# Kernel tuning notes

Hardware: AMD Instinct MI355X
Metric: run time of the kernel (lower is better)

## Reference

```python
import jax, jax.numpy as jnp
import numpy as np

B, F, D = 4096, 32, 32
LAYER_SIZE = [128, 128]


def setup_inputs() -> dict:
    key = jax.random.key(0)
    k1, k2, k3 = jax.random.split(key, 3)
    inputs = jax.random.normal(k1, (B, F, D), dtype=jnp.float32)
    # CIN filters: shape [1, field_nums[0]*field_nums[i], field_nums[i+1]]
    field_nums = [F] + LAYER_SIZE
    filter_0 = (jax.random.normal(k2, (1, field_nums[0] * field_nums[0], field_nums[1]), dtype=jnp.float32) * 0.05)
    filter_1 = (jax.random.normal(k3, (1, field_nums[0] * field_nums[1], field_nums[2]), dtype=jnp.float32) * 0.05)
    return {"inputs": inputs, "filter_0": filter_0, "filter_1": filter_1}


def _cin_forward(inputs, filters):
    x0 = inputs          # [B, F, D] -- hidden_nn_layers[0]
    prev = inputs        # hidden_nn_layers[-1]
    outs = []
    for W in filters:    # W: [1, F*M, N]
        # outer product over field dims: [B, F, M, D]
        z = jnp.einsum('bhd,bmd->bhmd', x0, prev)
        b, h, m, d = z.shape
        z = z.reshape(b, h * m, d)                 # [B, F*M, D]
        # 1x1 conv over the F*M axis == contraction with W[0]: [F*M, N]
        cur = jnp.einsum('bpd,pn->bnd', z, W[0])   # [B, N, D]
        cur = jax.nn.relu(cur)
        prev = cur
        outs.append(cur)
    result = jnp.concatenate(outs, axis=1)         # [B, sum(layer_size), D]
    return jnp.sum(result, axis=-1)                # [B, sum(layer_size)]


def reference(inputs, filter_0, filter_1):
    return _cin_forward(inputs, (filter_0, filter_1))
```

## Files before the change

### kernel.cpp

```cpp
#include <hip/hip_runtime.h>


typedef _Float16 half_t;
typedef _Float16 half4v __attribute__((ext_vector_type(4)));
typedef _Float16 half8 __attribute__((ext_vector_type(8)));
typedef float f32x16 __attribute__((ext_vector_type(16)));

__global__ void prep_w_kernel(const float* __restrict__ W0,
                              const float* __restrict__ W1,
                              half_t* __restrict__ Wp0,
                              half_t* __restrict__ Wp1) {
  int gid = blockIdx.x * 256 + threadIdx.x;
  int n = gid & 127;
  int tg = (gid >> 7) & 1;
  int s = gid >> 8;
  const float* W;
  half_t* Wp;
  int M, sl;
  if (s < 64) { W = W0; Wp = Wp0; M = 32; sl = s; }
  else        { W = W1; Wp = Wp1; M = 128; sl = s - 64; }
  int h = sl & 31, mc = sl >> 5;
  int kbase = h * M + mc * 16 + tg * 8;
  half8 v;
#pragma unroll
  for (int j = 0; j < 8; ++j) v[j] = (half_t)W[(size_t)(kbase + j) * 128 + n];
  *(half8*)(Wp + ((size_t)(sl * 2 + tg) * 128 + n) * 8) = v;
}

__device__ __forceinline__ int pswz(int row, int m) {
  return row * 128 + (((m >> 3) ^ (row & 15)) << 3) + (m & 7);
}

__device__ __forceinline__ f32x16 mfma3216(half8 a, half8 b, f32x16 c) {
  return __builtin_amdgcn_mfma_f32_32x32x16_f16(a, b, c, 0, 0, 0);
}

template <int MC, bool L1>
__device__ __forceinline__ void layer_loop(const half_t* __restrict__ Wp,
                                           const half_t* __restrict__ psrc,
                                           const half_t* __restrict__ xrd,
                                           int woff, int l31, int hi,
                                           f32x16 acc[2]) {
  half8 B0a = *(const half8*)(Wp + 0 * 2048 + woff);
  half8 B1a = *(const half8*)(Wp + 1 * 2048 + woff);
  half8 B0b = *(const half8*)(Wp + 2 * 2048 + woff);
  half8 B1b = *(const half8*)(Wp + 3 * 2048 + woff);
  half4v xqa = *(const half4v*)(xrd);
  half4v xqb = *(const half4v*)(xrd + 128);

  half8 P[2];
#pragma unroll
  for (int rt = 0; rt < 2; ++rt)
    P[rt] = L1 ? *(const half8*)&psrc[(rt * 32 + l31) * 40 + hi * 8]
               : *(const half8*)&psrc[pswz(rt * 32 + l31, hi * 8)];

#pragma unroll 1
  for (int mc = 0; mc < MC; ++mc) {
#pragma unroll 1
    for (int p = 0; p < 8; ++p) {
      const int g0 = mc * 16 + 2 * p;
#pragma unroll
      for (int rt = 0; rt < 2; ++rt)
        acc[rt] = mfma3216(P[rt] * xqa[rt * 2 + 0], B0a, acc[rt]);
#pragma unroll
      for (int rt = 0; rt < 2; ++rt)
        acc[rt] = mfma3216(P[rt] * xqa[rt * 2 + 1], B1a, acc[rt]);
      {
        const int sn = (2 * (g0 + 2)) & (MC * 32 - 1);
        B0a = *(const half8*)(Wp + (size_t)sn * 2048 + woff);
        B1a = *(const half8*)(Wp + (size_t)(sn + 1) * 2048 + woff);
        xqa = *(const half4v*)(xrd + ((2 * p + 2) & 15) * 128);
      }
#pragma unroll
      for (int rt = 0; rt < 2; ++rt)
        acc[rt] = mfma3216(P[rt] * xqb[rt * 2 + 0], B0b, acc[rt]);
#pragma unroll
      for (int rt = 0; rt < 2; ++rt)
        acc[rt] = mfma3216(P[rt] * xqb[rt * 2 + 1], B1b, acc[rt]);
      {
        const int sn = (2 * (g0 + 3)) & (MC * 32 - 1);
        B0b = *(const half8*)(Wp + (size_t)sn * 2048 + woff);
        B1b = *(const half8*)(Wp + (size_t)(sn + 1) * 2048 + woff);
        xqb = *(const half4v*)(xrd + ((2 * p + 3) & 15) * 128);
      }
    }
    if (mc + 1 < MC) {
      const int mn = (mc + 1) * 16;
#pragma unroll
      for (int rt = 0; rt < 2; ++rt)
        P[rt] = L1 ? *(const half8*)&psrc[(rt * 32 + l31) * 40 + mn + hi * 8]
                   : *(const half8*)&psrc[pswz(rt * 32 + l31, mn + hi * 8)];
    }
  }
}

__global__ __launch_bounds__(256, 6) void cin_fused_kernel(
    const float* __restrict__ x0,
    const half_t* __restrict__ Wp0,
    const half_t* __restrict__ Wp1,
    float* __restrict__ out) {
  __shared__ half_t xsf3[16 * 128];
  __shared__ half_t prevT[2 * 32 * 128];
  half_t* xT = prevT;

  const int tid = threadIdx.x;
  const int b0 = blockIdx.x * 2;

  const float4* x4 = (const float4*)(x0 + (size_t)b0 * 1024);
#pragma unroll
  for (int r = 0; r < 2; ++r) {
    int q = r * 256 + tid;
    float4 v = x4[q];
    int e = q * 4;
    int bi = e >> 10, h = (e >> 5) & 31, d0 = e & 31;
    half4v hv = {(half_t)v.x, (half_t)v.y, (half_t)v.z, (half_t)v.w};
#pragma unroll
    for (int j = 0; j < 4; ++j) {
      xsf3[(h >> 1) * 128 + (d0 + j) * 4 + bi * 2 + (h & 1)] = hv[j];
      xT[(bi * 32 + d0 + j) * 40 + h] = hv[j];
    }
  }
  __syncthreads();

  const int lane = tid & 63;
  const int l31 = lane & 31;
  const int hi = lane >> 5;
  const int wave = tid >> 6;
  const int n0 = wave * 32;

  const int woff = hi * 1024 + (n0 + l31) * 8;
  const half_t* xrd = &xsf3[l31 * 4];

  f32x16 acc[2];
#pragma unroll
  for (int rt = 0; rt < 2; ++rt)
#pragma unroll
    for (int r = 0; r < 16; ++r) acc[rt][r] = 0.f;

  layer_loop<2, true>(Wp0, xT, xrd, woff, l31, hi, acc);

  __syncthreads();

#pragma unroll
  for (int rt = 0; rt < 2; ++rt) {
    float s = 0.f;
#pragma unroll
    for (int r = 0; r < 16; ++r) {
      float v = acc[rt][r];
      v = v > 0.f ? v : 0.f;
      s += v;
      int d = (r & 3) + ((r >> 2) << 3) + hi * 4;
      prevT[pswz(rt * 32 + d, n0 + l31)] = (half_t)v;
      acc[rt][r] = 0.f;
    }
    s += __shfl_down(s, 32);
    if (lane < 32) out[(size_t)(b0 + rt) * 256 + n0 + lane] = s;
  }
  __syncthreads();

  layer_loop<8, false>(Wp1, prevT, xrd, woff, l31, hi, acc);

#pragma unroll
  for (int rt = 0; rt < 2; ++rt) {
    float s = 0.f;
#pragma unroll
    for (int r = 0; r < 16; ++r) {
      float v = acc[rt][r];
      s += v > 0.f ? v : 0.f;
    }
    s += __shfl_down(s, 32);
    if (lane < 32) out[(size_t)(b0 + rt) * 256 + 128 + n0 + lane] = s;
  }
}

extern "C" void kernel_launch(void* const* d_in, const int* in_sizes, int n_in,
                              void* d_out, int out_size, void* d_ws,
                              size_t ws_size, hipStream_t stream) {
  const float* x0 = (const float*)d_in[0];
  const float* w0 = (const float*)d_in[1];
  const float* w1 = (const float*)d_in[2];
  float* out = (float*)d_out;
  char* ws = (char*)d_ws;

  half_t* Wp0 = (half_t*)(ws);
  half_t* Wp1 = (half_t*)(ws + 64 * 2048 * 2);

  hipLaunchKernelGGL(prep_w_kernel, dim3(320), dim3(256), 0, stream, w0, w1,
                     Wp0, Wp1);
  hipLaunchKernelGGL(cin_fused_kernel, dim3(2048), dim3(256), 0, stream, x0,
                     Wp0, Wp1, out);
}
```

Before: 231.5 us.

## Process eight batch rows per block to reuse weight fragments across more MFMAs

Each block now handles 8 batch elements instead of 2, keeping 8 accumulator tiles per wave so that every loaded weight fragment feeds 8 MFMAs instead of 2. The x0 shared layout is split into two 4-batch halves read as half8 vectors per step, and the grid shrinks to 512 blocks with launch bounds lowered to 2 blocks per CU. This cuts global weight traffic per unit of work but raises register and LDS use, lowering occupancy and leaving fewer blocks than a large GPU has compute units to fill.

```diff
diff --git a/kernel.cpp b/kernel.cpp
--- a/kernel.cpp
+++ b/kernel.cpp
@@ -38,19 +38,18 @@
 template <int MC, bool L1>
 __device__ __forceinline__ void layer_loop(const half_t* __restrict__ Wp,
                                            const half_t* __restrict__ psrc,
-                                           const half_t* __restrict__ xrd,
+                                           const half_t* __restrict__ xAl,
+                                           const half_t* __restrict__ xBl,
                                            int woff, int l31, int hi,
-                                           f32x16 acc[2]) {
+                                           f32x16 acc[8]) {
   half8 B0a = *(const half8*)(Wp + 0 * 2048 + woff);
   half8 B1a = *(const half8*)(Wp + 1 * 2048 + woff);
   half8 B0b = *(const half8*)(Wp + 2 * 2048 + woff);
   half8 B1b = *(const half8*)(Wp + 3 * 2048 + woff);
-  half4v xqa = *(const half4v*)(xrd);
-  half4v xqb = *(const half4v*)(xrd + 128);
-
-  half8 P[2];
-#pragma unroll
-  for (int rt = 0; rt < 2; ++rt)
+
+  half8 P[8];
+#pragma unroll
+  for (int rt = 0; rt < 8; ++rt)
     P[rt] = L1 ? *(const half8*)&psrc[(rt * 32 + l31) * 40 + hi * 8]
                : *(const half8*)&psrc[pswz(rt * 32 + l31, hi * 8)];
 
@@ -59,64 +58,77 @@
 #pragma unroll 1
     for (int p = 0; p < 8; ++p) {
       const int g0 = mc * 16 + 2 * p;
-#pragma unroll
-      for (int rt = 0; rt < 2; ++rt)
-        acc[rt] = mfma3216(P[rt] * xqa[rt * 2 + 0], B0a, acc[rt]);
-#pragma unroll
-      for (int rt = 0; rt < 2; ++rt)
-        acc[rt] = mfma3216(P[rt] * xqa[rt * 2 + 1], B1a, acc[rt]);
+      half8 xLa = *(const half8*)(xAl + (2 * p) * 256);
+      half8 xHa = *(const half8*)(xBl + (2 * p) * 256);
+      half8 xLb = *(const half8*)(xAl + (2 * p + 1) * 256);
+      half8 xHb = *(const half8*)(xBl + (2 * p + 1) * 256);
+#pragma unroll
+      for (int rt = 0; rt < 8; ++rt) {
+        half_t xv = (rt < 4) ? xLa[(rt & 3) * 2 + 0] : xHa[(rt & 3) * 2 + 0];
+        acc[rt] = mfma3216(P[rt] * xv, B0a, acc[rt]);
+      }
+#pragma unroll
+      for (int rt = 0; rt < 8; ++rt) {
+        half_t xv = (rt < 4) ? xLa[(rt & 3) * 2 + 1] : xHa[(rt & 3) * 2 + 1];
+        acc[rt] = mfma3216(P[rt] * xv, B1a, acc[rt]);
+      }
       {
         const int sn = (2 * (g0 + 2)) & (MC * 32 - 1);
         B0a = *(const half8*)(Wp + (size_t)sn * 2048 + woff);
         B1a = *(const half8*)(Wp + (size_t)(sn + 1) * 2048 + woff);
-        xqa = *(const half4v*)(xrd + ((2 * p + 2) & 15) * 128);
-      }
-#pragma unroll
-      for (int rt = 0; rt < 2; ++rt)
-        acc[rt] = mfma3216(P[rt] * xqb[rt * 2 + 0], B0b, acc[rt]);
-#pragma unroll
-      for (int rt = 0; rt < 2; ++rt)
-        acc[rt] = mfma3216(P[rt] * xqb[rt * 2 + 1], B1b, acc[rt]);
+      }
+#pragma unroll
+      for (int rt = 0; rt < 8; ++rt) {
+        half_t xv = (rt < 4) ? xLb[(rt & 3) * 2 + 0] : xHb[(rt & 3) * 2 + 0];
+        acc[rt] = mfma3216(P[rt] * xv, B0b, acc[rt]);
+      }
+#pragma unroll
+      for (int rt = 0; rt < 8; ++rt) {
+        half_t xv = (rt < 4) ? xLb[(rt & 3) * 2 + 1] : xHb[(rt & 3) * 2 + 1];
+        acc[rt] = mfma3216(P[rt] * xv, B1b, acc[rt]);
+      }
       {
         const int sn = (2 * (g0 + 3)) & (MC * 32 - 1);
         B0b = *(const half8*)(Wp + (size_t)sn * 2048 + woff);
         B1b = *(const half8*)(Wp + (size_t)(sn + 1) * 2048 + woff);
-        xqb = *(const half4v*)(xrd + ((2 * p + 3) & 15) * 128);
       }
     }
     if (mc + 1 < MC) {
       const int mn = (mc + 1) * 16;
 #pragma unroll
-      for (int rt = 0; rt < 2; ++rt)
+      for (int rt = 0; rt < 8; ++rt)
         P[rt] = L1 ? *(const half8*)&psrc[(rt * 32 + l31) * 40 + mn + hi * 8]
                    : *(const half8*)&psrc[pswz(rt * 32 + l31, mn + hi * 8)];
     }
   }
 }
 
-__global__ __launch_bounds__(256, 6) void cin_fused_kernel(
+__global__ __launch_bounds__(256, 2) void cin_fused_kernel(
     const float* __restrict__ x0,
     const half_t* __restrict__ Wp0,
     const half_t* __restrict__ Wp1,
     float* __restrict__ out) {
-  __shared__ half_t xsf3[16 * 128];
-  __shared__ half_t prevT[2 * 32 * 128];
+  __shared__ half_t xA[16 * 32 * 8];
+  __shared__ half_t xB[16 * 32 * 8];
+  __shared__ half_t prevT[8 * 32 * 128];
   half_t* xT = prevT;
 
   const int tid = threadIdx.x;
-  const int b0 = blockIdx.x * 2;
+  const int b0 = blockIdx.x * 8;
 
   const float4* x4 = (const float4*)(x0 + (size_t)b0 * 1024);
 #pragma unroll
-  for (int r = 0; r < 2; ++r) {
+  for (int r = 0; r < 8; ++r) {
     int q = r * 256 + tid;
     float4 v = x4[q];
-    int e = q * 4;
-    int bi = e >> 10, h = (e >> 5) & 31, d0 = e & 31;
+    int e4 = q * 4;
+    int bi = e4 >> 10, h = (e4 >> 5) & 31, d0 = e4 & 31;
     half4v hv = {(half_t)v.x, (half_t)v.y, (half_t)v.z, (half_t)v.w};
+    half_t* xdst = (bi < 4) ? xA : xB;
+    const int bl = bi & 3;
 #pragma unroll
     for (int j = 0; j < 4; ++j) {
-      xsf3[(h >> 1) * 128 + (d0 + j) * 4 + bi * 2 + (h & 1)] = hv[j];
+      xdst[((h >> 1) * 32 + d0 + j) * 8 + bl * 2 + (h & 1)] = hv[j];
       xT[(bi * 32 + d0 + j) * 40 + h] = hv[j];
     }
   }
@@ -129,20 +141,21 @@
   const int n0 = wave * 32;
 
   const int woff = hi * 1024 + (n0 + l31) * 8;
-  const half_t* xrd = &xsf3[l31 * 4];
-
-  f32x16 acc[2];
-#pragma unroll
-  for (int rt = 0; rt < 2; ++rt)
+  const half_t* xAl = xA + l31 * 8;
+  const half_t* xBl = xB + l31 * 8;
+
+  f32x16 acc[8];
+#pragma unroll
+  for (int rt = 0; rt < 8; ++rt)
 #pragma unroll
     for (int r = 0; r < 16; ++r) acc[rt][r] = 0.f;
 
-  layer_loop<2, true>(Wp0, xT, xrd, woff, l31, hi, acc);
+  layer_loop<2, true>(Wp0, xT, xAl, xBl, woff, l31, hi, acc);
 
   __syncthreads();
 
 #pragma unroll
-  for (int rt = 0; rt < 2; ++rt) {
+  for (int rt = 0; rt < 8; ++rt) {
     float s = 0.f;
 #pragma unroll
     for (int r = 0; r < 16; ++r) {
@@ -158,10 +171,10 @@
   }
   __syncthreads();
 
-  layer_loop<8, false>(Wp1, prevT, xrd, woff, l31, hi, acc);
-
-#pragma unroll
-  for (int rt = 0; rt < 2; ++rt) {
+  layer_loop<8, false>(Wp1, prevT, xAl, xBl, woff, l31, hi, acc);
+
+#pragma unroll
+  for (int rt = 0; rt < 8; ++rt) {
     float s = 0.f;
 #pragma unroll
     for (int r = 0; r < 16; ++r) {
@@ -187,6 +200,6 @@
 
   hipLaunchKernelGGL(prep_w_kernel, dim3(320), dim3(256), 0, stream, w0, w1,
                      Wp0, Wp1);
-  hipLaunchKernelGGL(cin_fused_kernel, dim3(2048), dim3(256), 0, stream, x0,
+  hipLaunchKernelGGL(cin_fused_kernel, dim3(512), dim3(256), 0, stream, x0,
                      Wp0, Wp1, out);
 }
```

Result: faster. 200.7 us (-13.3%).
